# Performance work log

Hardware: AMD Instinct MI355X
Metric: run time of the kernel (lower is better)

The kernel has to match this reference:

```python
import jax, jax.numpy as jnp
import numpy as np


def setup_inputs() -> dict:
    key = jax.random.key(0)
    ks = jax.random.split(key, 5)
    B, D, U = 16384, 512, 512
    return {
        "inputs": jax.random.normal(ks[0], (B, D), dtype=jnp.float32),
        "h_prev": jax.random.normal(ks[1], (B, U), dtype=jnp.float32),
        "update_kernel": jax.random.normal(ks[2], (D + U, U), dtype=jnp.float32) * 0.03,
        "reset_kernel": jax.random.normal(ks[3], (D + U, U), dtype=jnp.float32) * 0.03,
        "hidden_kernel": jax.random.normal(ks[4], (D + U, U), dtype=jnp.float32) * 0.03,
        "update_bias": jnp.zeros((U,), dtype=jnp.float32),
        "reset_bias": jnp.zeros((U,), dtype=jnp.float32),
        "hidden_bias": jnp.zeros((U,), dtype=jnp.float32),
    }


def reference(inputs, h_prev, update_kernel, reset_kernel, hidden_kernel,
              update_bias, reset_bias, hidden_bias):
    # fused_input: [B, D+U]
    fused = jnp.concatenate([inputs, h_prev], axis=-1)
    zg = jax.nn.sigmoid(fused @ update_kernel + update_bias)   # update gate [B,U]
    rg = jax.nn.sigmoid(fused @ reset_kernel + reset_bias)     # reset gate  [B,U]
    h_tilde = jnp.tanh(
        jnp.concatenate([inputs, rg * h_prev], axis=-1) @ hidden_kernel + hidden_bias
    )
    ht = (1.0 - zg) * h_prev + zg * h_tilde
    return ht
```

## Files before the change

kernel.cpp:

```cpp
#include <hip/hip_runtime.h>
#include <hip/hip_bf16.h>
#include <math.h>

typedef __attribute__((ext_vector_type(4))) float f32x4;
typedef __attribute__((ext_vector_type(8))) float f32x8;
typedef __bf16 bf16x8 __attribute__((ext_vector_type(8)));
typedef unsigned short u16;
typedef u16 u16x8 __attribute__((ext_vector_type(8)));
typedef void __attribute__((address_space(1))) * as1p;
typedef void __attribute__((address_space(3))) * as3p;

__device__ __forceinline__ unsigned short f2bf(float f) {
    union { float f; unsigned int u; } v; v.f = f;
    unsigned int u = v.u;
    u += 0x7fffu + ((u >> 16) & 1u);
    return (unsigned short)(u >> 16);
}

__device__ __forceinline__ float bf2f(unsigned short b) {
    union { unsigned int u; float f; } v;
    v.u = ((unsigned int)b) << 16;
    return v.f;
}

__device__ __forceinline__ float fast_tanh(float v) {
    float vc = fminf(fmaxf(v, -15.f), 15.f);
    float e = __expf(2.f * vc);
    return (e - 1.f) / (e + 1.f);
}

__global__ void cvt_xh(const float* __restrict__ x, const float* __restrict__ h,
                       u16* __restrict__ xb, u16* __restrict__ hb, int n4) {
    int i = blockIdx.x * blockDim.x + threadIdx.x;
    int stride = gridDim.x * blockDim.x;
    const float4* x4 = (const float4*)x;
    const float4* h4 = (const float4*)h;
    ushort4* xb4 = (ushort4*)xb;
    ushort4* hb4 = (ushort4*)hb;
    for (; i < n4; i += stride) {
        float4 v = x4[i];
        xb4[i] = make_ushort4(f2bf(v.x), f2bf(v.y), f2bf(v.z), f2bf(v.w));
        float4 w = h4[i];
        hb4[i] = make_ushort4(f2bf(w.x), f2bf(w.y), f2bf(w.z), f2bf(w.w));
    }
}

__global__ void tr_cvt3(const float* __restrict__ s0, const float* __restrict__ s1,
                        const float* __restrict__ s2, u16* __restrict__ d0,
                        u16* __restrict__ d1, u16* __restrict__ d2) {
    __shared__ float t[32][33];
    const float* src = (blockIdx.z == 0) ? s0 : (blockIdx.z == 1) ? s1 : s2;
    u16* dst = (blockIdx.z == 0) ? d0 : (blockIdx.z == 1) ? d1 : d2;
    int n0 = blockIdx.x * 32;
    int k0 = blockIdx.y * 32;
    int tx = threadIdx.x, ty = threadIdx.y;
#pragma unroll
    for (int i = 0; i < 4; ++i)
        t[ty + i * 8][tx] = src[(size_t)(k0 + ty + i * 8) * 512 + n0 + tx];
    __syncthreads();
#pragma unroll
    for (int i = 0; i < 4; ++i)
        dst[(size_t)(n0 + ty + i * 8) * 1024 + k0 + tx] = f2bf(t[tx][ty + i * 8]);
}

__device__ __forceinline__ void stage_sw(const u16* g, int gstride, u16* lds, int tid) {
#pragma unroll
    for (int i = 0; i < 4; ++i) {
        int ob = i * 4096 + ((tid >> 6) << 10);
        int o = ob + ((tid & 63) << 4);
        int row = o >> 7;
        int cb = (o & 127) ^ ((row & 7) << 4);
        const u16* gp = g + (size_t)row * gstride + (cb >> 1);
        __builtin_amdgcn_global_load_lds((as1p)(void*)gp, (as3p)(void*)(lds + (ob >> 1)), 16, 0, 0);
    }
}

__device__ __forceinline__ bf16x8 ld_frag(const u16* region, int r, int kb) {
    int byte = (r << 7) + (kb ^ ((r & 7) << 4));
    return *(const bf16x8*)((const char*)region + byte);
}

__device__ __forceinline__ void compute_tile(const u16* LA, const u16* LB,
                                             int wr, int wc, int l, f32x4 (&acc)[4][4]) {
    int fr = l & 15;
    int kbb = (l >> 4) << 4;
#pragma unroll
    for (int q = 0; q < 2; ++q) {
        bf16x8 a[4], b[4];
#pragma unroll
        for (int m = 0; m < 4; ++m)
            a[m] = ld_frag(LA, wr * 64 + m * 16 + fr, q * 64 + kbb);
#pragma unroll
        for (int n = 0; n < 4; ++n)
            b[n] = ld_frag(LB, wc * 64 + n * 16 + fr, q * 64 + kbb);
#pragma unroll
        for (int m = 0; m < 4; ++m)
#pragma unroll
            for (int n = 0; n < 4; ++n)
                acc[m][n] = __builtin_amdgcn_mfma_f32_16x16x32_bf16(a[m], b[n], acc[m][n], 0, 0, 0);
    }
}

template<typename AF, typename BF>
__device__ __forceinline__ void kloop(AF ga, BF gb, u16* lds, int tid,
                                      int wr, int wc, int l, f32x4 (&acc)[4][4]) {
    stage_sw(ga(0), 512, lds, tid);
    stage_sw(gb(0), 1024, lds + 8192, tid);
    __syncthreads();
#pragma unroll
    for (int i = 0; i < 15; ++i) {
        u16* nxt = lds + ((i + 1) & 1) * 16384;
        const u16* cur = lds + (i & 1) * 16384;
        stage_sw(ga(i + 1), 512, nxt, tid);
        stage_sw(gb(i + 1), 1024, nxt + 8192, tid);
        compute_tile(cur, cur + 8192, wr, wc, l, acc);
        __syncthreads();
    }
    compute_tile(lds + 16384, lds + 16384 + 8192, wr, wc, l, acc);
}

__device__ __forceinline__ void scatter_acc(float* tf, const f32x4 (&acc)[4][4],
                                            int wr, int wc, int l) {
    int colb = wc * 64;
    int rowb = wr * 64 + ((l >> 4) << 2);
#pragma unroll
    for (int n = 0; n < 4; ++n) {
        int col = colb + n * 16 + (l & 15);
#pragma unroll
        for (int m = 0; m < 4; ++m) {
            int row0 = rowb + m * 16;
#pragma unroll
            for (int r = 0; r < 4; ++r)
                tf[(row0 + r) * 128 + col] = acc[m][n][r];
        }
    }
}

__global__ __launch_bounds__(256) void gz_k(
    const u16* __restrict__ Xb, const u16* __restrict__ Hb, const u16* __restrict__ Wt,
    const float* __restrict__ ub, u16* __restrict__ zgb) {
    __shared__ u16 lds[2 * 16384];
    int tid = threadIdx.x;
    int l = tid & 63, w = tid >> 6;
    int wr = w >> 1, wc = w & 1;
    int swz = (blockIdx.x & 7) * 64 + (blockIdx.x >> 3);
    int mb = swz >> 2, nb = swz & 3;
    int m0 = mb * 128, n0 = nb * 128;
    f32x4 acc[4][4];
#pragma unroll
    for (int m = 0; m < 4; ++m)
#pragma unroll
        for (int n = 0; n < 4; ++n) acc[m][n] = (f32x4){0.f, 0.f, 0.f, 0.f};

    auto ga = [&](int t) -> const u16* {
        return (t < 8) ? (Xb + (size_t)m0 * 512 + t * 64)
                       : (Hb + (size_t)m0 * 512 + (t - 8) * 64);
    };
    auto gb = [&](int t) -> const u16* { return Wt + (size_t)n0 * 1024 + t * 64; };
    kloop(ga, gb, lds, tid, wr, wc, l, acc);

    __syncthreads();
    float* tf = (float*)lds;
    scatter_acc(tf, acc, wr, wc, l);
    __syncthreads();
#pragma unroll
    for (int i = 0; i < 8; ++i) {
        int chunk = i * 256 + tid;
        int row = chunk >> 4;
        int c8 = (chunk & 15) << 3;
        const float* src = &tf[row * 128 + c8];
        int gcol = n0 + c8;
        u16x8 o;
#pragma unroll
        for (int j = 0; j < 8; ++j) {
            float v = src[j] + ub[gcol + j];
            o[j] = f2bf(1.f / (1.f + __expf(-v)));
        }
        *(u16x8*)&zgb[(size_t)(m0 + row) * 512 + gcol] = o;
    }
}

__global__ __launch_bounds__(256) void gr_k(
    const u16* __restrict__ Xb, const u16* __restrict__ Hb, const u16* __restrict__ Wt,
    const float* __restrict__ rb_, u16* __restrict__ rgh) {
    __shared__ u16 lds[2 * 16384];
    int tid = threadIdx.x;
    int l = tid & 63, w = tid >> 6;
    int wr = w >> 1, wc = w & 1;
    int swz = (blockIdx.x & 7) * 64 + (blockIdx.x >> 3);
    int mb = swz >> 2, nb = swz & 3;
    int m0 = mb * 128, n0 = nb * 128;
    f32x4 acc[4][4];
#pragma unroll
    for (int m = 0; m < 4; ++m)
#pragma unroll
        for (int n = 0; n < 4; ++n) acc[m][n] = (f32x4){0.f, 0.f, 0.f, 0.f};

    auto ga = [&](int t) -> const u16* {
        return (t < 8) ? (Xb + (size_t)m0 * 512 + t * 64)
                       : (Hb + (size_t)m0 * 512 + (t - 8) * 64);
    };
    auto gb = [&](int t) -> const u16* { return Wt + (size_t)n0 * 1024 + t * 64; };
    kloop(ga, gb, lds, tid, wr, wc, l, acc);

    __syncthreads();
    float* tf = (float*)lds;
    scatter_acc(tf, acc, wr, wc, l);
    __syncthreads();
#pragma unroll
    for (int i = 0; i < 8; ++i) {
        int chunk = i * 256 + tid;
        int row = chunk >> 4;
        int c8 = (chunk & 15) << 3;
        const float* src = &tf[row * 128 + c8];
        int gcol = n0 + c8;
        size_t gbase = (size_t)(m0 + row) * 512 + gcol;
        u16x8 h8 = *(const u16x8*)&Hb[gbase];
        u16x8 o;
#pragma unroll
        for (int j = 0; j < 8; ++j) {
            float v = src[j] + rb_[gcol + j];
            float s = 1.f / (1.f + __expf(-v));
            o[j] = f2bf(s * bf2f(h8[j]));
        }
        *(u16x8*)&rgh[gbase] = o;
    }
}

__global__ __launch_bounds__(256) void gh_k(
    const u16* __restrict__ Xb, const u16* __restrict__ rgh, const u16* __restrict__ Wt,
    const float* __restrict__ hp, const u16* __restrict__ zgb, const float* __restrict__ hb,
    float* __restrict__ out) {
    __shared__ u16 lds[2 * 16384];
    int tid = threadIdx.x;
    int l = tid & 63, w = tid >> 6;
    int wr = w >> 1, wc = w & 1;
    int swz = (blockIdx.x & 7) * 64 + (blockIdx.x >> 3);
    int mb = swz >> 2, nb = swz & 3;
    int m0 = mb * 128, n0 = nb * 128;
    f32x4 acc[4][4];
#pragma unroll
    for (int m = 0; m < 4; ++m)
#pragma unroll
        for (int n = 0; n < 4; ++n) acc[m][n] = (f32x4){0.f, 0.f, 0.f, 0.f};

    auto ga = [&](int t) -> const u16* {
        return (t < 8) ? (Xb + (size_t)m0 * 512 + t * 64)
                       : (rgh + (size_t)m0 * 512 + (t - 8) * 64);
    };
    auto gb = [&](int t) -> const u16* { return Wt + (size_t)n0 * 1024 + t * 64; };
    kloop(ga, gb, lds, tid, wr, wc, l, acc);

    __syncthreads();
    float* tf = (float*)lds;
    scatter_acc(tf, acc, wr, wc, l);
    __syncthreads();
#pragma unroll
    for (int i = 0; i < 8; ++i) {
        int chunk = i * 256 + tid;
        int row = chunk >> 4;
        int c8 = (chunk & 15) << 3;
        const float* src = &tf[row * 128 + c8];
        int gcol = n0 + c8;
        size_t gbase = (size_t)(m0 + row) * 512 + gcol;
        f32x8 h8 = *(const f32x8*)&hp[gbase];
        u16x8 z8 = *(const u16x8*)&zgb[gbase];
        f32x8 o;
#pragma unroll
        for (int j = 0; j < 8; ++j) {
            float v = src[j] + hb[gcol + j];
            float t = fast_tanh(v);
            float z = bf2f(z8[j]);
            o[j] = h8[j] + z * (t - h8[j]);
        }
        *(f32x8*)&out[gbase] = o;
    }
}

extern "C" void kernel_launch(void* const* d_in, const int* in_sizes, int n_in,
                              void* d_out, int out_size, void* d_ws, size_t ws_size,
                              hipStream_t stream) {
    const float* x  = (const float*)d_in[0];
    const float* h  = (const float*)d_in[1];
    const float* wz = (const float*)d_in[2];
    const float* wr = (const float*)d_in[3];
    const float* wh = (const float*)d_in[4];
    const float* ub = (const float*)d_in[5];
    const float* rb = (const float*)d_in[6];
    const float* hb = (const float*)d_in[7];
    float* out = (float*)d_out;

    const int B = 16384;
    char* ws = (char*)d_ws;
    size_t off = 0;
    u16* Xb  = (u16*)(ws + off); off += (size_t)B * 512 * 2;
    u16* Hb  = (u16*)(ws + off); off += (size_t)B * 512 * 2;
    u16* Wzt = (u16*)(ws + off); off += (size_t)512 * 1024 * 2;
    u16* Wrt = (u16*)(ws + off); off += (size_t)512 * 1024 * 2;
    u16* Wht = (u16*)(ws + off); off += (size_t)512 * 1024 * 2;
    u16* rgh = (u16*)(ws + off); off += (size_t)B * 512 * 2;
    u16* zgb = (u16*)(ws + off); off += (size_t)B * 512 * 2;

    cvt_xh<<<2048, 256, 0, stream>>>(x, h, Xb, Hb, B * 512 / 4);

    dim3 tb(32, 8), tg(16, 32, 3);
    tr_cvt3<<<tg, tb, 0, stream>>>(wz, wr, wh, Wzt, Wrt, Wht);

    gz_k<<<512, 256, 0, stream>>>(Xb, Hb, Wzt, ub, zgb);
    gr_k<<<512, 256, 0, stream>>>(Xb, Hb, Wrt, rb, rgh);
    gh_k<<<512, 256, 0, stream>>>(Xb, rgh, Wht, h, zgb, hb, out);
}
```

Measured before the change: 101.7 us.

## Fuse update-gate GEMM into hidden-state GEMM kernel, sharing the input A tiles

Drops the separate update-gate kernel and computes the update gate inside the final hidden kernel, which now holds two accumulator sets. Both GEMMs share the X half of the A operand, staged through a double-buffered K=32 loop with swizzled LDS loads. This removes one launch, the zgb bf16 round-trip through global memory and the duplicate X reads. The cost is doubled accumulator registers (launch bounds 256,2), an extra LDS scatter pass, and h_prev now read from its bf16 copy, which lowers precision.

New measurement: 98.58 us. -3.1%, faster.

```diff
diff --git a/kernel.cpp b/kernel.cpp
--- a/kernel.cpp
+++ b/kernel.cpp
@@ -136,50 +136,6 @@
     }
 }
 
-__global__ __launch_bounds__(256) void gz_k(
-    const u16* __restrict__ Xb, const u16* __restrict__ Hb, const u16* __restrict__ Wt,
-    const float* __restrict__ ub, u16* __restrict__ zgb) {
-    __shared__ u16 lds[2 * 16384];
-    int tid = threadIdx.x;
-    int l = tid & 63, w = tid >> 6;
-    int wr = w >> 1, wc = w & 1;
-    int swz = (blockIdx.x & 7) * 64 + (blockIdx.x >> 3);
-    int mb = swz >> 2, nb = swz & 3;
-    int m0 = mb * 128, n0 = nb * 128;
-    f32x4 acc[4][4];
-#pragma unroll
-    for (int m = 0; m < 4; ++m)
-#pragma unroll
-        for (int n = 0; n < 4; ++n) acc[m][n] = (f32x4){0.f, 0.f, 0.f, 0.f};
-
-    auto ga = [&](int t) -> const u16* {
-        return (t < 8) ? (Xb + (size_t)m0 * 512 + t * 64)
-                       : (Hb + (size_t)m0 * 512 + (t - 8) * 64);
-    };
-    auto gb = [&](int t) -> const u16* { return Wt + (size_t)n0 * 1024 + t * 64; };
-    kloop(ga, gb, lds, tid, wr, wc, l, acc);
-
-    __syncthreads();
-    float* tf = (float*)lds;
-    scatter_acc(tf, acc, wr, wc, l);
-    __syncthreads();
-#pragma unroll
-    for (int i = 0; i < 8; ++i) {
-        int chunk = i * 256 + tid;
-        int row = chunk >> 4;
-        int c8 = (chunk & 15) << 3;
-        const float* src = &tf[row * 128 + c8];
-        int gcol = n0 + c8;
-        u16x8 o;
-#pragma unroll
-        for (int j = 0; j < 8; ++j) {
-            float v = src[j] + ub[gcol + j];
-            o[j] = f2bf(1.f / (1.f + __expf(-v)));
-        }
-        *(u16x8*)&zgb[(size_t)(m0 + row) * 512 + gcol] = o;
-    }
-}
-
 __global__ __launch_bounds__(256) void gr_k(
     const u16* __restrict__ Xb, const u16* __restrict__ Hb, const u16* __restrict__ Wt,
     const float* __restrict__ rb_, u16* __restrict__ rgh) {
@@ -227,9 +183,27 @@
     }
 }
 
-__global__ __launch_bounds__(256) void gh_k(
-    const u16* __restrict__ Xb, const u16* __restrict__ rgh, const u16* __restrict__ Wt,
-    const float* __restrict__ hp, const u16* __restrict__ zgb, const float* __restrict__ hb,
+__device__ __forceinline__ void stage32(const u16* g, int gstride, u16* region, int tid) {
+#pragma unroll
+    for (int i = 0; i < 2; ++i) {
+        int ob = i * 4096 + ((tid >> 6) << 10);
+        int o = ob + ((tid & 63) << 4);
+        int row = o >> 6;
+        int cb = (o & 63) ^ ((row & 3) << 4);
+        const u16* gp = g + (size_t)row * gstride + (cb >> 1);
+        __builtin_amdgcn_global_load_lds((as1p)(void*)gp, (as3p)(void*)(region + (ob >> 1)), 16, 0, 0);
+    }
+}
+
+__device__ __forceinline__ bf16x8 ld32(const u16* region, int r, int kb) {
+    int byte = (r << 6) + (kb ^ ((r & 3) << 4));
+    return *(const bf16x8*)((const char*)region + byte);
+}
+
+__global__ __launch_bounds__(256, 2) void ghz_k(
+    const u16* __restrict__ Xb, const u16* __restrict__ Hb, const u16* __restrict__ rgh,
+    const u16* __restrict__ Wht, const u16* __restrict__ Wzt,
+    const float* __restrict__ ub, const float* __restrict__ hb,
     float* __restrict__ out) {
     __shared__ u16 lds[2 * 16384];
     int tid = threadIdx.x;
@@ -238,40 +212,106 @@
     int swz = (blockIdx.x & 7) * 64 + (blockIdx.x >> 3);
     int mb = swz >> 2, nb = swz & 3;
     int m0 = mb * 128, n0 = nb * 128;
-    f32x4 acc[4][4];
+
+    f32x4 acc_h[4][4], acc_z[4][4];
 #pragma unroll
     for (int m = 0; m < 4; ++m)
 #pragma unroll
-        for (int n = 0; n < 4; ++n) acc[m][n] = (f32x4){0.f, 0.f, 0.f, 0.f};
-
-    auto ga = [&](int t) -> const u16* {
-        return (t < 8) ? (Xb + (size_t)m0 * 512 + t * 64)
-                       : (rgh + (size_t)m0 * 512 + (t - 8) * 64);
+        for (int n = 0; n < 4; ++n) {
+            acc_h[m][n] = (f32x4){0.f, 0.f, 0.f, 0.f};
+            acc_z[m][n] = (f32x4){0.f, 0.f, 0.f, 0.f};
+        }
+
+    auto ah = [&](int t) -> const u16* {
+        return (t < 16) ? (Xb + (size_t)m0 * 512 + t * 32)
+                        : (rgh + (size_t)m0 * 512 + (t - 16) * 32);
     };
-    auto gb = [&](int t) -> const u16* { return Wt + (size_t)n0 * 1024 + t * 64; };
-    kloop(ga, gb, lds, tid, wr, wc, l, acc);
-
-    __syncthreads();
+    auto az = [&](int t) -> const u16* {
+        return Hb + (size_t)m0 * 512 + (t - 16) * 32;
+    };
+    auto bhp = [&](int t) -> const u16* { return Wht + (size_t)n0 * 1024 + t * 32; };
+    auto bzp = [&](int t) -> const u16* { return Wzt + (size_t)n0 * 1024 + t * 32; };
+
+    const int fr = l & 15;
+    const int kbb = (l >> 4) << 4;
+
+    stage32(ah(0), 512, lds, tid);
+    stage32(bhp(0), 1024, lds + 8192, tid);
+    stage32(bzp(0), 1024, lds + 12288, tid);
+    __syncthreads();
+
+#pragma unroll
+    for (int i = 0; i < 32; ++i) {
+        const u16* cur = lds + (i & 1) * 16384;
+        if (i < 31) {
+            u16* nxt = lds + ((i + 1) & 1) * 16384;
+            stage32(ah(i + 1), 512, nxt, tid);
+            if (i + 1 >= 16) stage32(az(i + 1), 512, nxt + 4096, tid);
+            stage32(bhp(i + 1), 1024, nxt + 8192, tid);
+            stage32(bzp(i + 1), 1024, nxt + 12288, tid);
+        }
+        const u16* Ahr = cur;
+        const u16* Azr = (i < 16) ? cur : (cur + 4096);
+        const u16* Bhr = cur + 8192;
+        const u16* Bzr = cur + 12288;
+        bf16x8 a[4], azf[4], bh4[4], bz4[4];
+#pragma unroll
+        for (int m = 0; m < 4; ++m) {
+            a[m]   = ld32(Ahr, wr * 64 + m * 16 + fr, kbb);
+            azf[m] = ld32(Azr, wr * 64 + m * 16 + fr, kbb);
+        }
+#pragma unroll
+        for (int n = 0; n < 4; ++n) {
+            bh4[n] = ld32(Bhr, wc * 64 + n * 16 + fr, kbb);
+            bz4[n] = ld32(Bzr, wc * 64 + n * 16 + fr, kbb);
+        }
+#pragma unroll
+        for (int m = 0; m < 4; ++m)
+#pragma unroll
+            for (int n = 0; n < 4; ++n) {
+                acc_h[m][n] = __builtin_amdgcn_mfma_f32_16x16x32_bf16(a[m], bh4[n], acc_h[m][n], 0, 0, 0);
+                acc_z[m][n] = __builtin_amdgcn_mfma_f32_16x16x32_bf16(azf[m], bz4[n], acc_z[m][n], 0, 0, 0);
+            }
+        __syncthreads();
+    }
+
     float* tf = (float*)lds;
-    scatter_acc(tf, acc, wr, wc, l);
-    __syncthreads();
+    scatter_acc(tf, acc_z, wr, wc, l);
+    __syncthreads();
+    u16x8 zreg[8];
 #pragma unroll
     for (int i = 0; i < 8; ++i) {
         int chunk = i * 256 + tid;
         int row = chunk >> 4;
         int c8 = (chunk & 15) << 3;
-        const float* src = &tf[row * 128 + c8];
+        f32x8 vz = *(const f32x8*)&tf[row * 128 + c8];
+        f32x8 ubv = *(const f32x8*)&ub[n0 + c8];
+#pragma unroll
+        for (int j = 0; j < 8; ++j) {
+            float s = 1.f / (1.f + __expf(-(vz[j] + ubv[j])));
+            zreg[i][j] = f2bf(s);
+        }
+    }
+    __syncthreads();
+    scatter_acc(tf, acc_h, wr, wc, l);
+    __syncthreads();
+#pragma unroll
+    for (int i = 0; i < 8; ++i) {
+        int chunk = i * 256 + tid;
+        int row = chunk >> 4;
+        int c8 = (chunk & 15) << 3;
         int gcol = n0 + c8;
         size_t gbase = (size_t)(m0 + row) * 512 + gcol;
-        f32x8 h8 = *(const f32x8*)&hp[gbase];
-        u16x8 z8 = *(const u16x8*)&zgb[gbase];
+        f32x8 vh = *(const f32x8*)&tf[row * 128 + c8];
+        f32x8 hbv = *(const f32x8*)&hb[gcol];
+        u16x8 h8 = *(const u16x8*)&Hb[gbase];
         f32x8 o;
 #pragma unroll
         for (int j = 0; j < 8; ++j) {
-            float v = src[j] + hb[gcol + j];
-            float t = fast_tanh(v);
-            float z = bf2f(z8[j]);
-            o[j] = h8[j] + z * (t - h8[j]);
+            float t = fast_tanh(vh[j] + hbv[j]);
+            float h0 = bf2f(h8[j]);
+            float z = bf2f(zreg[i][j]);
+            o[j] = h0 + z * (t - h0);
         }
         *(f32x8*)&out[gbase] = o;
     }
@@ -299,14 +339,12 @@
     u16* Wrt = (u16*)(ws + off); off += (size_t)512 * 1024 * 2;
     u16* Wht = (u16*)(ws + off); off += (size_t)512 * 1024 * 2;
     u16* rgh = (u16*)(ws + off); off += (size_t)B * 512 * 2;
-    u16* zgb = (u16*)(ws + off); off += (size_t)B * 512 * 2;
 
     cvt_xh<<<2048, 256, 0, stream>>>(x, h, Xb, Hb, B * 512 / 4);
 
     dim3 tb(32, 8), tg(16, 32, 3);
     tr_cvt3<<<tg, tb, 0, stream>>>(wz, wr, wh, Wzt, Wrt, Wht);
 
-    gz_k<<<512, 256, 0, stream>>>(Xb, Hb, Wzt, ub, zgb);
     gr_k<<<512, 256, 0, stream>>>(Xb, Hb, Wrt, rb, rgh);
-    gh_k<<<512, 256, 0, stream>>>(Xb, rgh, Wht, h, zgb, hb, out);
-}
+    ghz_k<<<512, 256, 0, stream>>>(Xb, Hb, rgh, Wht, Wzt, ub, hb, out);
+}
```

## Halve GEMM K-tile to shrink LDS, add occupancy hint, merge prep kernels

Applied to the files above, without the earlier changes.

The K step of the three bf16 GEMM kernels drops from 64 to 32, which halves the double-buffered LDS from 64KB to 32KB per block. The swizzle is adjusted to match, and launch_bounds(256,4) is added so more blocks can be resident per CU. The epilogue now scatters accumulators in two halves to fit the smaller LDS, and the bias loads are vectorized. The conversion and transpose prep kernels are merged into a single launch. In exchange there are twice as many K iterations and barriers, and the occupancy hint may force register spills.

After: 98.77 us. -2.9%, faster.

```diff
diff --git a/kernel.cpp b/kernel.cpp
--- a/kernel.cpp
+++ b/kernel.cpp
@@ -29,100 +29,104 @@
     return (e - 1.f) / (e + 1.f);
 }
 
-__global__ void cvt_xh(const float* __restrict__ x, const float* __restrict__ h,
-                       u16* __restrict__ xb, u16* __restrict__ hb, int n4) {
-    int i = blockIdx.x * blockDim.x + threadIdx.x;
-    int stride = gridDim.x * blockDim.x;
-    const float4* x4 = (const float4*)x;
-    const float4* h4 = (const float4*)h;
-    ushort4* xb4 = (ushort4*)xb;
-    ushort4* hb4 = (ushort4*)hb;
-    for (; i < n4; i += stride) {
-        float4 v = x4[i];
-        xb4[i] = make_ushort4(f2bf(v.x), f2bf(v.y), f2bf(v.z), f2bf(v.w));
-        float4 w = h4[i];
-        hb4[i] = make_ushort4(f2bf(w.x), f2bf(w.y), f2bf(w.z), f2bf(w.w));
-    }
-}
-
-__global__ void tr_cvt3(const float* __restrict__ s0, const float* __restrict__ s1,
-                        const float* __restrict__ s2, u16* __restrict__ d0,
-                        u16* __restrict__ d1, u16* __restrict__ d2) {
+__global__ void prep_k(const float* __restrict__ x, const float* __restrict__ h,
+                       const float* __restrict__ wz, const float* __restrict__ wrr,
+                       const float* __restrict__ wh,
+                       u16* __restrict__ xb, u16* __restrict__ hb,
+                       u16* __restrict__ wzt, u16* __restrict__ wrt, u16* __restrict__ wht) {
     __shared__ float t[32][33];
-    const float* src = (blockIdx.z == 0) ? s0 : (blockIdx.z == 1) ? s1 : s2;
-    u16* dst = (blockIdx.z == 0) ? d0 : (blockIdx.z == 1) ? d1 : d2;
-    int n0 = blockIdx.x * 32;
-    int k0 = blockIdx.y * 32;
-    int tx = threadIdx.x, ty = threadIdx.y;
-#pragma unroll
-    for (int i = 0; i < 4; ++i)
-        t[ty + i * 8][tx] = src[(size_t)(k0 + ty + i * 8) * 512 + n0 + tx];
-    __syncthreads();
-#pragma unroll
-    for (int i = 0; i < 4; ++i)
-        dst[(size_t)(n0 + ty + i * 8) * 1024 + k0 + tx] = f2bf(t[tx][ty + i * 8]);
-}
-
-__device__ __forceinline__ void stage_sw(const u16* g, int gstride, u16* lds, int tid) {
-#pragma unroll
-    for (int i = 0; i < 4; ++i) {
+    int bid = blockIdx.x;
+    int tid = threadIdx.x;
+    if (bid < 2048) {
+        const int n4 = 16384 * 512 / 4;
+        int i = bid * 256 + tid;
+        const int stride = 2048 * 256;
+        const float4* x4 = (const float4*)x;
+        const float4* h4 = (const float4*)h;
+        ushort4* xb4 = (ushort4*)xb;
+        ushort4* hb4 = (ushort4*)hb;
+        for (; i < n4; i += stride) {
+            float4 v = x4[i];
+            xb4[i] = make_ushort4(f2bf(v.x), f2bf(v.y), f2bf(v.z), f2bf(v.w));
+            float4 w = h4[i];
+            hb4[i] = make_ushort4(f2bf(w.x), f2bf(w.y), f2bf(w.z), f2bf(w.w));
+        }
+    } else {
+        int b = bid - 2048;
+        int z = b >> 9;
+        int rem = b & 511;
+        const float* src = (z == 0) ? wz : (z == 1) ? wrr : wh;
+        u16* dst = (z == 0) ? wzt : (z == 1) ? wrt : wht;
+        int n0 = (rem & 15) * 32;
+        int k0 = (rem >> 4) * 32;
+        int tx = tid & 31, ty = tid >> 5;
+#pragma unroll
+        for (int i = 0; i < 4; ++i)
+            t[ty + i * 8][tx] = src[(size_t)(k0 + ty + i * 8) * 512 + n0 + tx];
+        __syncthreads();
+#pragma unroll
+        for (int i = 0; i < 4; ++i)
+            dst[(size_t)(n0 + ty + i * 8) * 1024 + k0 + tx] = f2bf(t[tx][ty + i * 8]);
+    }
+}
+
+__device__ __forceinline__ void stage32(const u16* g, int gstride, u16* region, int tid) {
+#pragma unroll
+    for (int i = 0; i < 2; ++i) {
         int ob = i * 4096 + ((tid >> 6) << 10);
         int o = ob + ((tid & 63) << 4);
-        int row = o >> 7;
-        int cb = (o & 127) ^ ((row & 7) << 4);
+        int row = o >> 6;
+        int cb = (o & 63) ^ ((row & 3) << 4);
         const u16* gp = g + (size_t)row * gstride + (cb >> 1);
-        __builtin_amdgcn_global_load_lds((as1p)(void*)gp, (as3p)(void*)(lds + (ob >> 1)), 16, 0, 0);
-    }
-}
-
-__device__ __forceinline__ bf16x8 ld_frag(const u16* region, int r, int kb) {
-    int byte = (r << 7) + (kb ^ ((r & 7) << 4));
+        __builtin_amdgcn_global_load_lds((as1p)(void*)gp, (as3p)(void*)(region + (ob >> 1)), 16, 0, 0);
+    }
+}
+
+__device__ __forceinline__ bf16x8 ld32(const u16* region, int r, int kb) {
+    int byte = (r << 6) + (kb ^ ((r & 3) << 4));
     return *(const bf16x8*)((const char*)region + byte);
 }
 
-__device__ __forceinline__ void compute_tile(const u16* LA, const u16* LB,
-                                             int wr, int wc, int l, f32x4 (&acc)[4][4]) {
+__device__ __forceinline__ void compute32(const u16* LA, const u16* LB,
+                                          int wr, int wc, int l, f32x4 (&acc)[4][4]) {
     int fr = l & 15;
     int kbb = (l >> 4) << 4;
-#pragma unroll
-    for (int q = 0; q < 2; ++q) {
-        bf16x8 a[4], b[4];
-#pragma unroll
-        for (int m = 0; m < 4; ++m)
-            a[m] = ld_frag(LA, wr * 64 + m * 16 + fr, q * 64 + kbb);
+    bf16x8 a[4], b[4];
+#pragma unroll
+    for (int m = 0; m < 4; ++m)
+        a[m] = ld32(LA, wr * 64 + m * 16 + fr, kbb);
+#pragma unroll
+    for (int n = 0; n < 4; ++n)
+        b[n] = ld32(LB, wc * 64 + n * 16 + fr, kbb);
+#pragma unroll
+    for (int m = 0; m < 4; ++m)
 #pragma unroll
         for (int n = 0; n < 4; ++n)
-            b[n] = ld_frag(LB, wc * 64 + n * 16 + fr, q * 64 + kbb);
-#pragma unroll
-        for (int m = 0; m < 4; ++m)
-#pragma unroll
-            for (int n = 0; n < 4; ++n)
-                acc[m][n] = __builtin_amdgcn_mfma_f32_16x16x32_bf16(a[m], b[n], acc[m][n], 0, 0, 0);
-    }
+            acc[m][n] = __builtin_amdgcn_mfma_f32_16x16x32_bf16(a[m], b[n], acc[m][n], 0, 0, 0);
 }
 
 template<typename AF, typename BF>
-__device__ __forceinline__ void kloop(AF ga, BF gb, u16* lds, int tid,
-                                      int wr, int wc, int l, f32x4 (&acc)[4][4]) {
-    stage_sw(ga(0), 512, lds, tid);
-    stage_sw(gb(0), 1024, lds + 8192, tid);
+__device__ __forceinline__ void kloop32(AF ga, BF gb, u16* lds, int tid,
+                                        int wr, int wc, int l, f32x4 (&acc)[4][4]) {
+    stage32(ga(0), 512, lds, tid);
+    stage32(gb(0), 1024, lds + 4096, tid);
     __syncthreads();
 #pragma unroll
-    for (int i = 0; i < 15; ++i) {
-        u16* nxt = lds + ((i + 1) & 1) * 16384;
-        const u16* cur = lds + (i & 1) * 16384;
-        stage_sw(ga(i + 1), 512, nxt, tid);
-        stage_sw(gb(i + 1), 1024, nxt + 8192, tid);
-        compute_tile(cur, cur + 8192, wr, wc, l, acc);
-        __syncthreads();
-    }
-    compute_tile(lds + 16384, lds + 16384 + 8192, wr, wc, l, acc);
-}
-
-__device__ __forceinline__ void scatter_acc(float* tf, const f32x4 (&acc)[4][4],
-                                            int wr, int wc, int l) {
+    for (int i = 0; i < 31; ++i) {
+        u16* nxt = lds + ((i + 1) & 1) * 8192;
+        const u16* cur = lds + (i & 1) * 8192;
+        stage32(ga(i + 1), 512, nxt, tid);
+        stage32(gb(i + 1), 1024, nxt + 4096, tid);
+        compute32(cur, cur + 4096, wr, wc, l, acc);
+        __syncthreads();
+    }
+    compute32(lds + 8192, lds + 8192 + 4096, wr, wc, l, acc);
+}
+
+__device__ __forceinline__ void scatter_half(float* tf, const f32x4 (&acc)[4][4],
+                                             int wc, int l) {
     int colb = wc * 64;
-    int rowb = wr * 64 + ((l >> 4) << 2);
+    int rowb = (l >> 4) << 2;
 #pragma unroll
     for (int n = 0; n < 4; ++n) {
         int col = colb + n * 16 + (l & 15);
@@ -136,10 +140,10 @@
     }
 }
 
-__global__ __launch_bounds__(256) void gz_k(
+__global__ __launch_bounds__(256, 4) void gz_k(
     const u16* __restrict__ Xb, const u16* __restrict__ Hb, const u16* __restrict__ Wt,
     const float* __restrict__ ub, u16* __restrict__ zgb) {
-    __shared__ u16 lds[2 * 16384];
+    __shared__ u16 lds[2 * 8192];
     int tid = threadIdx.x;
     int l = tid & 63, w = tid >> 6;
     int wr = w >> 1, wc = w & 1;
@@ -153,37 +157,39 @@
         for (int n = 0; n < 4; ++n) acc[m][n] = (f32x4){0.f, 0.f, 0.f, 0.f};
 
     auto ga = [&](int t) -> const u16* {
-        return (t < 8) ? (Xb + (size_t)m0 * 512 + t * 64)
-                       : (Hb + (size_t)m0 * 512 + (t - 8) * 64);
+        return (t < 16) ? (Xb + (size_t)m0 * 512 + t * 32)
+                        : (Hb + (size_t)m0 * 512 + (t - 16) * 32);
     };
-    auto gb = [&](int t) -> const u16* { return Wt + (size_t)n0 * 1024 + t * 64; };
-    kloop(ga, gb, lds, tid, wr, wc, l, acc);
-
-    __syncthreads();
+    auto gb = [&](int t) -> const u16* { return Wt + (size_t)n0 * 1024 + t * 32; };
+    kloop32(ga, gb, lds, tid, wr, wc, l, acc);
+
     float* tf = (float*)lds;
-    scatter_acc(tf, acc, wr, wc, l);
-    __syncthreads();
-#pragma unroll
-    for (int i = 0; i < 8; ++i) {
-        int chunk = i * 256 + tid;
-        int row = chunk >> 4;
-        int c8 = (chunk & 15) << 3;
-        const float* src = &tf[row * 128 + c8];
-        int gcol = n0 + c8;
-        u16x8 o;
-#pragma unroll
-        for (int j = 0; j < 8; ++j) {
-            float v = src[j] + ub[gcol + j];
-            o[j] = f2bf(1.f / (1.f + __expf(-v)));
-        }
-        *(u16x8*)&zgb[(size_t)(m0 + row) * 512 + gcol] = o;
-    }
-}
-
-__global__ __launch_bounds__(256) void gr_k(
+#pragma unroll
+    for (int half = 0; half < 2; ++half) {
+        __syncthreads();
+        if (wr == half) scatter_half(tf, acc, wc, l);
+        __syncthreads();
+#pragma unroll
+        for (int it = 0; it < 4; ++it) {
+            int chunk = it * 256 + tid;
+            int row = chunk >> 4;
+            int c8 = (chunk & 15) << 3;
+            f32x8 v8 = *(const f32x8*)&tf[row * 128 + c8];
+            int gcol = n0 + c8;
+            f32x8 ubv = *(const f32x8*)&ub[gcol];
+            u16x8 o;
+#pragma unroll
+            for (int j = 0; j < 8; ++j)
+                o[j] = f2bf(1.f / (1.f + __expf(-(v8[j] + ubv[j]))));
+            *(u16x8*)&zgb[(size_t)(m0 + half * 64 + row) * 512 + gcol] = o;
+        }
+    }
+}
+
+__global__ __launch_bounds__(256, 4) void gr_k(
     const u16* __restrict__ Xb, const u16* __restrict__ Hb, const u16* __restrict__ Wt,
     const float* __restrict__ rb_, u16* __restrict__ rgh) {
-    __shared__ u16 lds[2 * 16384];
+    __shared__ u16 lds[2 * 8192];
     int tid = threadIdx.x;
     int l = tid & 63, w = tid >> 6;
     int wr = w >> 1, wc = w & 1;
@@ -197,41 +203,44 @@
         for (int n = 0; n < 4; ++n) acc[m][n] = (f32x4){0.f, 0.f, 0.f, 0.f};
 
     auto ga = [&](int t) -> const u16* {
-        return (t < 8) ? (Xb + (size_t)m0 * 512 + t * 64)
-                       : (Hb + (size_t)m0 * 512 + (t - 8) * 64);
+        return (t < 16) ? (Xb + (size_t)m0 * 512 + t * 32)
+                        : (Hb + (size_t)m0 * 512 + (t - 16) * 32);
     };
-    auto gb = [&](int t) -> const u16* { return Wt + (size_t)n0 * 1024 + t * 64; };
-    kloop(ga, gb, lds, tid, wr, wc, l, acc);
-
-    __syncthreads();
+    auto gb = [&](int t) -> const u16* { return Wt + (size_t)n0 * 1024 + t * 32; };
+    kloop32(ga, gb, lds, tid, wr, wc, l, acc);
+
     float* tf = (float*)lds;
-    scatter_acc(tf, acc, wr, wc, l);
-    __syncthreads();
-#pragma unroll
-    for (int i = 0; i < 8; ++i) {
-        int chunk = i * 256 + tid;
-        int row = chunk >> 4;
-        int c8 = (chunk & 15) << 3;
-        const float* src = &tf[row * 128 + c8];
-        int gcol = n0 + c8;
-        size_t gbase = (size_t)(m0 + row) * 512 + gcol;
-        u16x8 h8 = *(const u16x8*)&Hb[gbase];
-        u16x8 o;
-#pragma unroll
-        for (int j = 0; j < 8; ++j) {
-            float v = src[j] + rb_[gcol + j];
-            float s = 1.f / (1.f + __expf(-v));
-            o[j] = f2bf(s * bf2f(h8[j]));
-        }
-        *(u16x8*)&rgh[gbase] = o;
-    }
-}
-
-__global__ __launch_bounds__(256) void gh_k(
+#pragma unroll
+    for (int half = 0; half < 2; ++half) {
+        __syncthreads();
+        if (wr == half) scatter_half(tf, acc, wc, l);
+        __syncthreads();
+#pragma unroll
+        for (int it = 0; it < 4; ++it) {
+            int chunk = it * 256 + tid;
+            int row = chunk >> 4;
+            int c8 = (chunk & 15) << 3;
+            f32x8 v8 = *(const f32x8*)&tf[row * 128 + c8];
+            int gcol = n0 + c8;
+            size_t gbase = (size_t)(m0 + half * 64 + row) * 512 + gcol;
+            f32x8 rbv = *(const f32x8*)&rb_[gcol];
+            u16x8 h8 = *(const u16x8*)&Hb[gbase];
+            u16x8 o;
+#pragma unroll
+            for (int j = 0; j < 8; ++j) {
+                float s = 1.f / (1.f + __expf(-(v8[j] + rbv[j])));
+                o[j] = f2bf(s * bf2f(h8[j]));
+            }
+            *(u16x8*)&rgh[gbase] = o;
+        }
+    }
+}
+
+__global__ __launch_bounds__(256, 4) void gh_k(
     const u16* __restrict__ Xb, const u16* __restrict__ rgh, const u16* __restrict__ Wt,
     const float* __restrict__ hp, const u16* __restrict__ zgb, const float* __restrict__ hb,
     float* __restrict__ out) {
-    __shared__ u16 lds[2 * 16384];
+    __shared__ u16 lds[2 * 8192];
     int tid = threadIdx.x;
     int l = tid & 63, w = tid >> 6;
     int wr = w >> 1, wc = w & 1;
@@ -245,35 +254,38 @@
         for (int n = 0; n < 4; ++n) acc[m][n] = (f32x4){0.f, 0.f, 0.f, 0.f};
 
     auto ga = [&](int t) -> const u16* {
-        return (t < 8) ? (Xb + (size_t)m0 * 512 + t * 64)
-                       : (rgh + (size_t)m0 * 512 + (t - 8) * 64);
+        return (t < 16) ? (Xb + (size_t)m0 * 512 + t * 32)
+                        : (rgh + (size_t)m0 * 512 + (t - 16) * 32);
     };
-    auto gb = [&](int t) -> const u16* { return Wt + (size_t)n0 * 1024 + t * 64; };
-    kloop(ga, gb, lds, tid, wr, wc, l, acc);
-
-    __syncthreads();
+    auto gb = [&](int t) -> const u16* { return Wt + (size_t)n0 * 1024 + t * 32; };
+    kloop32(ga, gb, lds, tid, wr, wc, l, acc);
+
     float* tf = (float*)lds;
-    scatter_acc(tf, acc, wr, wc, l);
-    __syncthreads();
-#pragma unroll
-    for (int i = 0; i < 8; ++i) {
-        int chunk = i * 256 + tid;
-        int row = chunk >> 4;
-        int c8 = (chunk & 15) << 3;
-        const float* src = &tf[row * 128 + c8];
-        int gcol = n0 + c8;
-        size_t gbase = (size_t)(m0 + row) * 512 + gcol;
-        f32x8 h8 = *(const f32x8*)&hp[gbase];
-        u16x8 z8 = *(const u16x8*)&zgb[gbase];
-        f32x8 o;
-#pragma unroll
-        for (int j = 0; j < 8; ++j) {
-            float v = src[j] + hb[gcol + j];
-            float t = fast_tanh(v);
-            float z = bf2f(z8[j]);
-            o[j] = h8[j] + z * (t - h8[j]);
-        }
-        *(f32x8*)&out[gbase] = o;
+#pragma unroll
+    for (int half = 0; half < 2; ++half) {
+        __syncthreads();
+        if (wr == half) scatter_half(tf, acc, wc, l);
+        __syncthreads();
+#pragma unroll
+        for (int it = 0; it < 4; ++it) {
+            int chunk = it * 256 + tid;
+            int row = chunk >> 4;
+            int c8 = (chunk & 15) << 3;
+            f32x8 v8 = *(const f32x8*)&tf[row * 128 + c8];
+            int gcol = n0 + c8;
+            size_t gbase = (size_t)(m0 + half * 64 + row) * 512 + gcol;
+            f32x8 hbv = *(const f32x8*)&hb[gcol];
+            f32x8 h8 = *(const f32x8*)&hp[gbase];
+            u16x8 z8 = *(const u16x8*)&zgb[gbase];
+            f32x8 o;
+#pragma unroll
+            for (int j = 0; j < 8; ++j) {
+                float t = fast_tanh(v8[j] + hbv[j]);
+                float z = bf2f(z8[j]);
+                o[j] = h8[j] + z * (t - h8[j]);
+            }
+            *(f32x8*)&out[gbase] = o;
+        }
     }
 }
 
@@ -301,10 +313,7 @@
     u16* rgh = (u16*)(ws + off); off += (size_t)B * 512 * 2;
     u16* zgb = (u16*)(ws + off); off += (size_t)B * 512 * 2;
 
-    cvt_xh<<<2048, 256, 0, stream>>>(x, h, Xb, Hb, B * 512 / 4);
-
-    dim3 tb(32, 8), tg(16, 32, 3);
-    tr_cvt3<<<tg, tb, 0, stream>>>(wz, wr, wh, Wzt, Wrt, Wht);
+    prep_k<<<2048 + 1536, 256, 0, stream>>>(x, h, wz, wr, wh, Xb, Hb, Wzt, Wrt, Wht);
 
     gz_k<<<512, 256, 0, stream>>>(Xb, Hb, Wzt, ub, zgb);
     gr_k<<<512, 256, 0, stream>>>(Xb, Hb, Wrt, rb, rgh);
```
